# Kernel optimization log

Hardware: AMD Instinct MI355X
Metric: run time of the kernel (lower is better)

## Reference

```python
import jax, jax.numpy as jnp
import numpy as np

SCALES = [1, 2, 4, 8]
NB_CODE = 1024
CODE_DIM = 512


def _linear_upsample(x, t_out):
    """torch F.interpolate(mode='linear', align_corners=False) on last axis. x: [N, C, t_in]."""
    t_in = x.shape[-1]
    if t_in == t_out:
        return x
    pos = (jnp.arange(t_out, dtype=x.dtype) + 0.5) * (t_in / t_out) - 0.5
    pos = jnp.clip(pos, 0.0, t_in - 1)
    lo = jnp.floor(pos).astype(jnp.int32)
    hi = jnp.minimum(lo + 1, t_in - 1)
    w = (pos - lo.astype(x.dtype))
    return x[..., lo] * (1.0 - w) + x[..., hi] * w


def setup_inputs() -> dict:
    key = jax.random.key(0)
    k1, k2 = jax.random.split(key)
    x = jax.random.normal(k1, (16, CODE_DIM, 2048), dtype=jnp.float32)
    codebook = jax.random.normal(k2, (NB_CODE, CODE_DIM), dtype=jnp.float32) * 0.02
    return {"x": x, "codebook": codebook}


def reference(x, codebook):
    # Eval-mode forward of HRQuantizeEMAReset: hierarchical residual VQ.
    # temperature=0 -> deterministic nearest-code argmax; m_lens=None -> full mask.
    N, C, T = x.shape
    residual = x
    f_hat = jnp.zeros_like(x)
    mean_vq_loss = jnp.asarray(0.0, dtype=x.dtype)
    csq = jnp.sum(codebook ** 2, axis=-1)  # [K]
    all_idx = []
    for scale in SCALES:
        t_s = T // scale
        # area downsample == average pooling over non-overlapping windows
        rest_down = residual if scale == 1 else residual.reshape(N, C, t_s, scale).mean(-1)
        flat = rest_down.transpose(0, 2, 1).reshape(N * t_s, C)  # (n t) c
        # squared-euclidean distance to all codes via GEMM
        dist = (jnp.sum(flat ** 2, axis=-1, keepdims=True)
                - 2.0 * flat @ codebook.T + csq[None, :])  # [N*t_s, K]
        code_idx = jnp.argmin(dist, axis=-1)  # gumbel_sample with temp=0
        all_idx.append(code_idx)
        x_d = codebook[code_idx].reshape(N, t_s, C).transpose(0, 2, 1)  # [N, C, t_s]
        up_x_d = _linear_upsample(x_d, T)
        residual = residual - up_x_d
        f_hat = f_hat + up_x_d
        # per-scale commitment loss against running reconstruction (detached)
        mean_vq_loss = mean_vq_loss + jnp.mean((x - jax.lax.stop_gradient(f_hat)) ** 2)
    mean_vq_loss = mean_vq_loss / len(SCALES)
    # straight-through estimator
    f_hat = x + jax.lax.stop_gradient(f_hat - x)
    # perplexity over all codes used across scales
    codes = jnp.concatenate(all_idx)
    counts = jnp.zeros((NB_CODE,), dtype=x.dtype).at[codes].add(1.0)
    prob = counts / jnp.sum(counts)
    perplexity = jnp.exp(-jnp.sum(prob * jnp.log(prob + 1e-7)))
    return f_hat, mean_vq_loss, perplexity
```

## Files before the change

kernel.cpp:

```cpp
#include <hip/hip_runtime.h>

#define CDIM 512
#define TDIM 2048
#define KCODE 1024
#define NTOT 16
#define FH_ELEMS (NTOT * CDIM * TDIM)
#define M_TOTAL 61440

typedef unsigned long long u64;
typedef unsigned int u32;
typedef __attribute__((ext_vector_type(8))) short s16x8;
typedef __attribute__((ext_vector_type(4))) float f32x4;
typedef __attribute__((ext_vector_type(4))) int i32x4;
typedef __attribute__((ext_vector_type(2))) int i32x2;

__device__ __forceinline__ u64 umin64(u64 a, u64 b) { return a < b ? a : b; }

__device__ __forceinline__ u32 bf16_rne(float f) {
  u32 u = __float_as_uint(f);
  return (u + 0x7fffu + ((u >> 16) & 1u)) >> 16;
}
__device__ __forceinline__ u32 pack2ch(float v0, float v1) {
  return bf16_rne(v0) | (bf16_rne(v1) << 16);
}
__device__ __forceinline__ int tile_addr(int ml, int kbyte) {
  return (ml * 128 + kbyte) ^ ((ml & 7) << 4);
}
__device__ __forceinline__ int iclamp(int v, int lo, int hi) {
  return v < lo ? lo : (v > hi ? hi : v);
}

__global__ __launch_bounds__(64) void csq_kernel(const float* __restrict__ cb,
                                                 float* __restrict__ csq) {
  const int code = blockIdx.x;
  const int t = threadIdx.x;
  const float* row = cb + (size_t)code * CDIM;
  float s = 0.f;
#pragma unroll
  for (int q = 0; q < 2; ++q) {
    float4 v = *(const float4*)(row + (t * 2 + q) * 4);
    s += v.x * v.x + v.y * v.y + v.z * v.z + v.w * v.w;
  }
#pragma unroll
  for (int off = 32; off; off >>= 1) s += __shfl_down(s, off, 64);
  if (t == 0) csq[code] = s;
}

__global__ __launch_bounds__(256) void cbprep_kernel(const float* __restrict__ cb,
                                                     char* __restrict__ cb_pack) {
  const int g = blockIdx.x * 256 + threadIdx.x;
  const int tile = g >> 10;
  const int L = (g & 1023) * 16;
  const int nt = tile >> 3, kc = tile & 7;
  const int code_local = L >> 7;
  const int kbyte = (L & 127) ^ ((code_local & 7) << 4);
  const int code = nt * 128 + code_local;
  const int c0 = kc * 64 + (kbyte >> 1);
  f32x4 va = *(const f32x4*)(cb + (size_t)code * CDIM + c0);
  f32x4 vb = *(const f32x4*)(cb + (size_t)code * CDIM + c0 + 4);
  i32x4 o = {(int)pack2ch(va[0], va[1]), (int)pack2ch(va[2], va[3]),
             (int)pack2ch(vb[0], vb[1]), (int)pack2ch(vb[2], vb[3])};
  *(i32x4*)(cb_pack + (size_t)g * 16) = o;
}

__global__ __launch_bounds__(256) void xprep_kernel(const float* __restrict__ x,
                                                    char* __restrict__ a1) {
  const int tid = threadIdx.x;
  const int lane = tid & 63, cq = tid >> 6;
  const int blk = blockIdx.x;
  const int tb = blk & 7;
  const int kc = (blk >> 3) & 7;
  const int n = blk >> 6;
  const int c0 = kc * 64 + cq * 16;
  const int t0 = tb * 256 + lane * 4;
  const float* xp = x + (size_t)n * (CDIM * TDIM) + (size_t)c0 * TDIM + t0;
  u32 pk[4][8];
#pragma unroll
  for (int jp = 0; jp < 8; ++jp) {
    f32x4 v0 = *(const f32x4*)(xp + (size_t)(2 * jp) * TDIM);
    f32x4 v1 = *(const f32x4*)(xp + (size_t)(2 * jp + 1) * TDIM);
#pragma unroll
    for (int tt = 0; tt < 4; ++tt) pk[tt][jp] = pack2ch(v0[tt], v1[tt]);
  }
  const int kbyte = cq * 32;
#pragma unroll
  for (int tt = 0; tt < 4; ++tt) {
    const int m = n * TDIM + t0 + tt;
    const size_t tbase = ((size_t)((m >> 7) * 8 + kc)) << 14;
    i32x4 o1 = {(int)pk[tt][0], (int)pk[tt][1], (int)pk[tt][2], (int)pk[tt][3]};
    i32x4 o2 = {(int)pk[tt][4], (int)pk[tt][5], (int)pk[tt][6], (int)pk[tt][7]};
    *(i32x4*)(a1 + tbase + tile_addr(m & 127, kbyte)) = o1;
    *(i32x4*)(a1 + tbase + tile_addr(m & 127, kbyte + 16)) = o2;
  }
}

__global__ __launch_bounds__(512, 2) void gemm_argmin_packed(
    const char* __restrict__ a_pack,
    const char* __restrict__ cb_pack,
    const float* __restrict__ csq,
    u64* __restrict__ packed) {
  __shared__ __align__(16) char smem[131072 + 1024];
  float* csq_s = (float*)(smem + 131072);

  const int id = blockIdx.x;
  const int nxq = gridDim.x >> 5;
  const int xcd = id & 7;
  const int rr = id >> 3;
  const int bx = xcd * nxq + (rr >> 2);
  const int by = rr & 3;

  const int tid = threadIdx.x;
  const int lane = tid & 63;
  const int w = tid >> 6;
  const int wc = w >> 2;
  const int wm = w & 3;
  const int row_base = bx * 256;
  const int code_base = by * 256;
  if (tid < 256) csq_s[tid] = csq[code_base + tid];

  const f32x4 zero = {0.f, 0.f, 0.f, 0.f};
  f32x4 acc[8][4];
#pragma unroll
  for (int fc = 0; fc < 8; ++fc)
#pragma unroll
    for (int fm = 0; fm < 4; ++fm) acc[fc][fm] = zero;

  const size_t aBase = ((size_t)(bx * 2) * 8) << 14;
  const size_t bBase = ((size_t)(by * 2) * 8) << 14;

  auto stage = [&](int buf, int kc) {
    char* dst = smem + buf * 65536;
    const char* gA0 = a_pack + aBase + ((size_t)kc << 14);
    const char* gA1 = a_pack + aBase + ((size_t)(8 + kc) << 14);
    const char* gB0 = cb_pack + bBase + ((size_t)kc << 14);
    const char* gB1 = cb_pack + bBase + ((size_t)(8 + kc) << 14);
    const int o = tid * 16;
#pragma unroll
    for (int p = 0; p < 2; ++p) {
      const int q = o + p * 8192;
      __builtin_amdgcn_global_load_lds(
          (const __attribute__((address_space(1))) u32*)(gA0 + q),
          (__attribute__((address_space(3))) u32*)(dst + q), 16, 0, 0);
      __builtin_amdgcn_global_load_lds(
          (const __attribute__((address_space(1))) u32*)(gA1 + q),
          (__attribute__((address_space(3))) u32*)(dst + 16384 + q), 16, 0, 0);
      __builtin_amdgcn_global_load_lds(
          (const __attribute__((address_space(1))) u32*)(gB0 + q),
          (__attribute__((address_space(3))) u32*)(dst + 32768 + q), 16, 0, 0);
      __builtin_amdgcn_global_load_lds(
          (const __attribute__((address_space(1))) u32*)(gB1 + q),
          (__attribute__((address_space(3))) u32*)(dst + 49152 + q), 16, 0, 0);
    }
  };

  stage(0, 0);
  __syncthreads();

  int cur = 0;
  for (int kc = 0; kc < 8; ++kc) {
    if (kc < 7) stage(cur ^ 1, kc + 1);
    const char* X = smem + cur * 65536;
    const char* C = X + 32768;
#pragma unroll
    for (int ks = 0; ks < 2; ++ks) {
      const int kb = ks * 64 + (lane >> 4) * 16;
      s16x8 af[8], bq[4];
#pragma unroll
      for (int fc = 0; fc < 8; ++fc) {
        const int cr = wc * 128 + fc * 16 + (lane & 15);
        af[fc] = *(const s16x8*)(C + ((cr >> 7) << 14) +
                                 tile_addr(cr & 127, kb));
      }
#pragma unroll
      for (int fm = 0; fm < 4; ++fm) {
        const int mr = wm * 64 + fm * 16 + (lane & 15);
        bq[fm] = *(const s16x8*)(X + ((mr >> 7) << 14) +
                                 tile_addr(mr & 127, kb));
      }
      __builtin_amdgcn_s_setprio(1);
#pragma unroll
      for (int fc = 0; fc < 8; ++fc)
#pragma unroll
        for (int fm = 0; fm < 4; ++fm)
          acc[fc][fm] = __builtin_amdgcn_mfma_f32_16x16x32_bf16(
              af[fc], bq[fm], acc[fc][fm], 0, 0, 0);
      __builtin_amdgcn_s_setprio(0);
    }
    __syncthreads();
    cur ^= 1;
  }

  u64 best[4] = {~0ull, ~0ull, ~0ull, ~0ull};
#pragma unroll
  for (int fc = 0; fc < 8; ++fc) {
#pragma unroll
    for (int r4 = 0; r4 < 4; ++r4) {
      const int cl = wc * 128 + fc * 16 + (lane >> 4) * 4 + r4;
      const float cs = csq_s[cl];
      const u64 codebits = (u32)(code_base + cl);
#pragma unroll
      for (int fm = 0; fm < 4; ++fm) {
        float d = fmaf(-2.0f, acc[fc][fm][r4], cs);
        u32 u = __float_as_uint(d);
        u = (u & 0x80000000u) ? ~u : (u | 0x80000000u);
        best[fm] = umin64(best[fm], ((u64)u << 32) | codebits);
      }
    }
  }
#pragma unroll
  for (int fm = 0; fm < 4; ++fm) {
    u64 b = best[fm];
#pragma unroll
    for (int off = 16; off < 64; off <<= 1) {
      u32 lo = (u32)b, hi = (u32)(b >> 32);
      lo = (u32)__shfl_xor((int)lo, off, 64);
      hi = (u32)__shfl_xor((int)hi, off, 64);
      b = umin64(b, ((u64)hi << 32) | lo);
    }
    if ((lane >> 4) == 0)
      atomicMin(&packed[row_base + wm * 64 + fm * 16 + (lane & 15)], b);
  }
}

__global__ __launch_bounds__(256) void pack2_kernel(
    const float* __restrict__ x, const float* __restrict__ cb,
    const u64* __restrict__ packed, char* __restrict__ a2,
    float* __restrict__ poolr2) {
  __shared__ float rows1[16][516];
  __shared__ int idx1[16];
  const int tid = threadIdx.x;
  const int blk = blockIdx.x;
  const int n = blk >> 7;
  const int tau0 = (blk & 127) * 8;
  const int tb = tau0 * 2;
  if (tid < 16)
    idx1[tid] = (int)(packed[(size_t)n * TDIM + tb + tid] & 0xffffffffull);
  __syncthreads();
  {
    const int rj = tid >> 4, c16 = tid & 15;
    const float* src = cb + (size_t)idx1[rj] * CDIM;
#pragma unroll
    for (int q = 0; q < 8; ++q) {
      const int c = c16 * 4 + q * 64;
      *(f32x4*)&rows1[rj][c] = *(const f32x4*)(src + c);
    }
  }
  __syncthreads();

  const int cg = tid >> 1, half = tid & 1;
  const int c0 = cg * 4;
  const int tl0 = half * 8;
  const size_t xbase =
      (size_t)n * (CDIM * TDIM) + (size_t)c0 * TDIM + tb + tl0;

  f32x4 ru[8];
#pragma unroll
  for (int t = 0; t < 8; ++t) ru[t] = *(const f32x4*)&rows1[tl0 + t][c0];

  float p2[4][4];
#pragma unroll
  for (int j = 0; j < 4; ++j) {
    f32x4 xa = *(const f32x4*)(x + xbase + (size_t)j * TDIM);
    f32x4 xb = *(const f32x4*)(x + xbase + (size_t)j * TDIM + 4);
#pragma unroll
    for (int q = 0; q < 4; ++q) {
      const float e0 = (q < 2) ? xa[2 * q] : xb[2 * q - 4];
      const float e1 = (q < 2) ? xa[2 * q + 1] : xb[2 * q - 3];
      const float r0 = e0 - ru[2 * q][j];
      const float r1 = e1 - ru[2 * q + 1][j];
      p2[j][q] = (r0 + r1) * 0.5f;
    }
  }
#pragma unroll
  for (int q = 0; q < 4; ++q) {
    f32x4 o = {p2[0][q], p2[1][q], p2[2][q], p2[3][q]};
    *(f32x4*)(poolr2 + (size_t)n * (1024 * CDIM) +
              (size_t)(tau0 + half * 4 + q) * CDIM + c0) = o;
  }
  const int kc = c0 >> 6, kbyte = (c0 & 63) * 2;
#pragma unroll
  for (int q = 0; q < 4; ++q) {
    const int m = n * 1024 + tau0 + half * 4 + q;
    i32x2 o = {(int)pack2ch(p2[0][q], p2[1][q]),
               (int)pack2ch(p2[2][q], p2[3][q])};
    *(i32x2*)(a2 + (((size_t)((m >> 7) * 8 + kc)) << 14) +
              tile_addr(m & 127, kbyte)) = o;
  }
}

template <int TP, bool WPOOL>
__global__ __launch_bounds__(256) void packN_kernel(
    const float* __restrict__ pin, const float* __restrict__ cb,
    const u64* __restrict__ packed, char* __restrict__ a_next,
    float* __restrict__ pout) {
  constexpr int OFF = (TP == 1024) ? 32768 : 49152;
  constexpr int TILES = TP / 16;
  constexpr int TO = TP / 2;
  __shared__ float rows[18][516];
  __shared__ int idxs[18];
  const int tid = threadIdx.x;
  const int blk = blockIdx.x;
  const int n = blk / TILES;
  const int o0 = (blk % TILES) * 8;
  const int s0 = o0 * 2;
  if (tid < 18) {
    const int sig = iclamp(s0 - 1 + tid, 0, TP - 1);
    idxs[tid] = (int)(packed[OFF + (size_t)n * TP + sig] & 0xffffffffull);
  }
  __syncthreads();
  for (int j = 0; j < 18; ++j) {
    const int c = tid * 2;
    const float* src = cb + (size_t)idxs[j] * CDIM + c;
    rows[j][c] = src[0];
    rows[j][c + 1] = src[1];
  }
  __syncthreads();

  const int cg = tid >> 1, half = tid & 1;
  const int c0 = cg * 4;
  f32x4 inv[8];
#pragma unroll
  for (int l = 0; l < 8; ++l)
    inv[l] = *(const f32x4*)(pin + (size_t)n * (TP * CDIM) +
                             (size_t)(s0 + half * 8 + l) * CDIM + c0);

  float pv[4][4];
#pragma unroll
  for (int q = 0; q < 4; ++q) {
    const int e = half * 8 + 2 * q;
    const int sa = e + 1, sb = e + 2;
    f32x4 Rm = *(const f32x4*)&rows[sa - 1][c0];
    f32x4 Rc = *(const f32x4*)&rows[sa][c0];
    f32x4 Rp = *(const f32x4*)&rows[sb][c0];
    f32x4 Rpp = *(const f32x4*)&rows[sb + 1][c0];
    f32x4 ua = 0.125f * (Rm + Rp) + 0.75f * Rc;
    f32x4 ub = 0.125f * (Rc + Rpp) + 0.75f * Rp;
#pragma unroll
    for (int j = 0; j < 4; ++j)
      pv[j][q] = ((inv[2 * q][j] - ua[j]) + (inv[2 * q + 1][j] - ub[j])) * 0.5f;
  }

  if constexpr (WPOOL) {
#pragma unroll
    for (int q = 0; q < 4; ++q) {
      f32x4 o = {pv[0][q], pv[1][q], pv[2][q], pv[3][q]};
      *(f32x4*)(pout + (size_t)n * (TO * CDIM) +
                (size_t)(o0 + half * 4 + q) * CDIM + c0) = o;
    }
  }
  const int kc = c0 >> 6, kbyte = (c0 & 63) * 2;
#pragma unroll
  for (int q = 0; q < 4; ++q) {
    const int m = n * TO + o0 + half * 4 + q;
    i32x2 o = {(int)pack2ch(pv[0][q], pv[1][q]),
               (int)pack2ch(pv[2][q], pv[3][q])};
    *(i32x2*)(a_next + (((size_t)((m >> 7) * 8 + kc)) << 14) +
              tile_addr(m & 127, kbyte)) = o;
  }
}

__global__ __launch_bounds__(256) void final_kernel(
    const float* __restrict__ x, float* __restrict__ out,
    const float* __restrict__ cb, const u64* __restrict__ packed,
    float* __restrict__ lossPart) {
  __shared__ float red[4];
  const int tid = threadIdx.x;
  const int blk = blockIdx.x;
  const int ch = blk & 1;
  const int t0 = ((blk >> 1) & 127) * 16;
  const int n = blk >> 8;
  const int cg = tid >> 2, qt = tid & 3;
  const int c0 = ch * 256 + cg * 4;
  const int tb = t0 + qt * 4;

  const u64* ip1 = packed + (size_t)n * TDIM;
  const u64* ip2 = packed + 32768 + (size_t)n * 1024;
  const u64* ip4 = packed + 49152 + (size_t)n * 512;
  const u64* ip8 = packed + 57344 + (size_t)n * 256;

  f32x4 R1[4], R2[4], R4[3], R8[2];
#pragma unroll
  for (int k = 0; k < 4; ++k)
    R1[k] = *(const f32x4*)(
        cb + (size_t)(u32)(ip1[tb + k] & 0xffffffffull) * CDIM + c0);
  const int b2 = tb >> 1;
#pragma unroll
  for (int k = 0; k < 4; ++k) {
    const int s = iclamp(b2 - 1 + k, 0, 1023);
    R2[k] = *(const f32x4*)(
        cb + (size_t)(u32)(ip2[s] & 0xffffffffull) * CDIM + c0);
  }
  const int b4 = tb >> 2;
#pragma unroll
  for (int k = 0; k < 3; ++k) {
    const int s = iclamp(b4 - 1 + k, 0, 511);
    R4[k] = *(const f32x4*)(
        cb + (size_t)(u32)(ip4[s] & 0xffffffffull) * CDIM + c0);
  }
  const int b8 = (tb >> 3) - 1 + ((tb >> 2) & 1);
#pragma unroll
  for (int k = 0; k < 2; ++k) {
    const int s = iclamp(b8 + k, 0, 255);
    R8[k] = *(const f32x4*)(
        cb + (size_t)(u32)(ip8[s] & 0xffffffffull) * CDIM + c0);
  }

  const size_t xbase = (size_t)n * (CDIM * TDIM) + (size_t)c0 * TDIM + tb;
  f32x4 xa[4], fa[4];
#pragma unroll
  for (int j = 0; j < 4; ++j)
    xa[j] = *(const f32x4*)(x + xbase + (size_t)j * TDIM);

  const int s2n[4] = {0, 1, 1, 2};
  const float w2n[4] = {0.75f, 0.25f, 0.75f, 0.25f};
  const int s4n[4] = {0, 0, 1, 1};
  const float w4n[4] = {0.625f, 0.875f, 0.125f, 0.375f};
  const float w8base = (tb & 4) ? 0.0625f : 0.5625f;

  float ss1 = 0.f, ss2 = 0.f, ss3 = 0.f, ss4 = 0.f;
#pragma unroll
  for (int tt = 0; tt < 4; ++tt) {
    f32x4 u2 = R2[s2n[tt]] * (1.f - w2n[tt]) + R2[s2n[tt] + 1] * w2n[tt];
    f32x4 u4 = R4[s4n[tt]] * (1.f - w4n[tt]) + R4[s4n[tt] + 1] * w4n[tt];
    const float w8 = w8base + tt * 0.125f;
    f32x4 u8 = R8[0] * (1.f - w8) + R8[1] * w8;
    f32x4 xv;
#pragma unroll
    for (int j = 0; j < 4; ++j) xv[j] = xa[j][tt];
    f32x4 r1 = xv - R1[tt];
    f32x4 r2 = r1 - u2;
    f32x4 r3 = r2 - u4;
    f32x4 r4 = r3 - u8;
#pragma unroll
    for (int j = 0; j < 4; ++j) {
      ss1 += r1[j] * r1[j];
      ss2 += r2[j] * r2[j];
      ss3 += r3[j] * r3[j];
      ss4 += r4[j] * r4[j];
    }
    f32x4 fh = xv - r4;
#pragma unroll
    for (int j = 0; j < 4; ++j) fa[j][tt] = fh[j];
  }
#pragma unroll
  for (int j = 0; j < 4; ++j)
    *(f32x4*)(out + xbase + (size_t)j * TDIM) = fa[j];

  __shared__ float red2[4][4];
  float sv[4] = {ss1, ss2, ss3, ss4};
  const int w = tid >> 6, lane = tid & 63;
#pragma unroll
  for (int st = 0; st < 4; ++st) {
    float v = sv[st];
#pragma unroll
    for (int off = 32; off; off >>= 1) v += __shfl_down(v, off, 64);
    if (lane == 0) red2[w][st] = v;
  }
  __syncthreads();
  if (tid < 4)
    lossPart[tid * 4096 + blk] =
        red2[0][tid] + red2[1][tid] + red2[2][tid] + red2[3][tid];
  (void)red;
}

__global__ __launch_bounds__(256) void hist_kernel(const u64* __restrict__ packed,
                                                   int* __restrict__ hist) {
  const int i = blockIdx.x * 256 + threadIdx.x;
  const int code = (int)(packed[i] & 0xFFFFFFFFull);
  atomicAdd(&hist[code], 1);
}

__global__ __launch_bounds__(256) void finalize_kernel(
    const float* __restrict__ lossPart, const int* __restrict__ hist,
    float* __restrict__ outTail) {
  __shared__ float red[4];
  const int tid = threadIdx.x;
  float s = 0.f;
  for (int i = tid; i < 4 * 4096; i += 256) s += lossPart[i];
#pragma unroll
  for (int off = 32; off; off >>= 1) s += __shfl_down(s, off, 64);
  if ((tid & 63) == 0) red[tid >> 6] = s;
  __syncthreads();
  const float loss =
      (red[0] + red[1] + red[2] + red[3]) * (1.0f / (4.0f * 16777216.0f));
  __syncthreads();
  float e = 0.f;
  for (int k = tid; k < KCODE; k += 256) {
    float p = (float)hist[k] * (1.0f / 61440.0f);
    e += p * logf(p + 1e-7f);
  }
#pragma unroll
  for (int off = 32; off; off >>= 1) e += __shfl_down(e, off, 64);
  if ((tid & 63) == 0) red[tid >> 6] = e;
  __syncthreads();
  if (tid == 0) {
    outTail[0] = loss;
    outTail[1] = expf(-(red[0] + red[1] + red[2] + red[3]));
  }
}

extern "C" void kernel_launch(void* const* d_in, const int* in_sizes, int n_in,
                              void* d_out, int out_size, void* d_ws,
                              size_t ws_size, hipStream_t stream) {
  const float* x = (const float*)d_in[0];
  const float* cb = (const float*)d_in[1];
  float* out = (float*)d_out;

  char* ws = (char*)d_ws;
  u64* packed = (u64*)ws;
  float* csq = (float*)(ws + 491520);
  int* hist = (int*)(ws + 495616);
  float* lossPart = (float*)(ws + 499712);
  char* cb_pack = ws + 565248;
  char* a2 = ws + (2ull << 20);
  char* a4 = ws + (18ull << 20);
  char* a8 = ws + (26ull << 20);

  hipMemsetAsync(packed, 0xFF, (size_t)M_TOTAL * 8, stream);
  hipMemsetAsync(hist, 0, KCODE * sizeof(int), stream);
  csq_kernel<<<KCODE, 64, 0, stream>>>(cb, csq);
  cbprep_kernel<<<256, 256, 0, stream>>>(cb, cb_pack);

  u64* p1 = packed;
  u64* p2 = packed + 32768;
  u64* p4 = packed + 49152;
  u64* p8 = packed + 57344;

  char* a1 = (char*)out;
  float* poolr2 = out;
  float* poolr4 = out + 8388608;

  xprep_kernel<<<1024, 256, 0, stream>>>(x, a1);
  gemm_argmin_packed<<<128 * 4, 512, 0, stream>>>(a1, cb_pack, csq, p1);
  pack2_kernel<<<2048, 256, 0, stream>>>(x, cb, packed, a2, poolr2);
  gemm_argmin_packed<<<64 * 4, 512, 0, stream>>>(a2, cb_pack, csq, p2);
  packN_kernel<1024, true>
      <<<1024, 256, 0, stream>>>(poolr2, cb, packed, a4, poolr4);
  gemm_argmin_packed<<<32 * 4, 512, 0, stream>>>(a4, cb_pack, csq, p4);
  packN_kernel<512, false>
      <<<512, 256, 0, stream>>>(poolr4, cb, packed, a8, nullptr);
  gemm_argmin_packed<<<16 * 4, 512, 0, stream>>>(a8, cb_pack, csq, p8);
  final_kernel<<<4096, 256, 0, stream>>>(x, out, cb, packed, lossPart);

  hist_kernel<<<240, 256, 0, stream>>>(packed, hist);
  finalize_kernel<<<1, 256, 0, stream>>>(lossPart, hist, out + FH_ELEMS);
}
```

Baseline: 247.6 us.

## Restructure pack kernels to channel-major pooled layout with direct codebook gathers

Rewrites pack2 and packN so each wave covers 256 time steps for 4 channels, reading codebook rows straight from global memory instead of staging them in shared memory. The intermediate pooled residual buffers switch from time-major to channel-major so reads and writes along time are coalesced. Blocks are remapped with a chunked swizzle of block IDs, pack2 launches twice as many blocks, and final_kernel gets the same wave/lane-to-(time, channel) mapping. The aim is to remove LDS staging and barriers and improve coalescing, at the cost of more scattered 16-byte codebook gathers through cache.

```diff
diff --git a/kernel.cpp b/kernel.cpp
--- a/kernel.cpp
+++ b/kernel.cpp
@@ -11,6 +11,7 @@
 typedef unsigned int u32;
 typedef __attribute__((ext_vector_type(8))) short s16x8;
 typedef __attribute__((ext_vector_type(4))) float f32x4;
+typedef __attribute__((ext_vector_type(2))) float f32x2;
 typedef __attribute__((ext_vector_type(4))) int i32x4;
 typedef __attribute__((ext_vector_type(2))) int i32x2;
 
@@ -28,6 +29,9 @@
 }
 __device__ __forceinline__ int iclamp(int v, int lo, int hi) {
   return v < lo ? lo : (v > hi ? hi : v);
+}
+__device__ __forceinline__ int swz_chunk(int b, int nblk) {
+  return (b & 7) * (nblk >> 3) + (b >> 3);
 }
 
 __global__ __launch_bounds__(64) void csq_kernel(const float* __restrict__ cb,
@@ -226,61 +230,45 @@
     const float* __restrict__ x, const float* __restrict__ cb,
     const u64* __restrict__ packed, char* __restrict__ a2,
     float* __restrict__ poolr2) {
-  __shared__ float rows1[16][516];
-  __shared__ int idx1[16];
   const int tid = threadIdx.x;
-  const int blk = blockIdx.x;
-  const int n = blk >> 7;
-  const int tau0 = (blk & 127) * 8;
-  const int tb = tau0 * 2;
-  if (tid < 16)
-    idx1[tid] = (int)(packed[(size_t)n * TDIM + tb + tid] & 0xffffffffull);
-  __syncthreads();
-  {
-    const int rj = tid >> 4, c16 = tid & 15;
-    const float* src = cb + (size_t)idx1[rj] * CDIM;
-#pragma unroll
-    for (int q = 0; q < 8; ++q) {
-      const int c = c16 * 4 + q * 64;
-      *(f32x4*)&rows1[rj][c] = *(const f32x4*)(src + c);
-    }
-  }
-  __syncthreads();
-
-  const int cg = tid >> 1, half = tid & 1;
-  const int c0 = cg * 4;
-  const int tl0 = half * 8;
-  const size_t xbase =
-      (size_t)n * (CDIM * TDIM) + (size_t)c0 * TDIM + tb + tl0;
-
-  f32x4 ru[8];
-#pragma unroll
-  for (int t = 0; t < 8; ++t) ru[t] = *(const f32x4*)&rows1[tl0 + t][c0];
-
-  float p2[4][4];
+  const int w = tid >> 6, lane = tid & 63;
+  const int L = swz_chunk(blockIdx.x, gridDim.x);
+  const int cbk = L & 31;
+  const int tt = (L >> 5) & 7;
+  const int n = L >> 8;
+  const int c0 = cbk * 16 + w * 4;
+  const int tb = tt * 256 + lane * 4;
+  const int tau0 = tb >> 1;
+
+  const u64* ip1 = packed + (size_t)n * TDIM;
+  f32x4 R1[4];
+#pragma unroll
+  for (int k = 0; k < 4; ++k)
+    R1[k] = *(const f32x4*)(
+        cb + (size_t)(u32)(ip1[tb + k] & 0xffffffffull) * CDIM + c0);
+
+  const size_t xbase = (size_t)n * (CDIM * TDIM) + (size_t)c0 * TDIM + tb;
+  float p2[4][2];
 #pragma unroll
   for (int j = 0; j < 4; ++j) {
     f32x4 xa = *(const f32x4*)(x + xbase + (size_t)j * TDIM);
-    f32x4 xb = *(const f32x4*)(x + xbase + (size_t)j * TDIM + 4);
-#pragma unroll
-    for (int q = 0; q < 4; ++q) {
-      const float e0 = (q < 2) ? xa[2 * q] : xb[2 * q - 4];
-      const float e1 = (q < 2) ? xa[2 * q + 1] : xb[2 * q - 3];
-      const float r0 = e0 - ru[2 * q][j];
-      const float r1 = e1 - ru[2 * q + 1][j];
+#pragma unroll
+    for (int q = 0; q < 2; ++q) {
+      const float r0 = xa[2 * q] - R1[2 * q][j];
+      const float r1 = xa[2 * q + 1] - R1[2 * q + 1][j];
       p2[j][q] = (r0 + r1) * 0.5f;
     }
   }
 #pragma unroll
-  for (int q = 0; q < 4; ++q) {
-    f32x4 o = {p2[0][q], p2[1][q], p2[2][q], p2[3][q]};
-    *(f32x4*)(poolr2 + (size_t)n * (1024 * CDIM) +
-              (size_t)(tau0 + half * 4 + q) * CDIM + c0) = o;
+  for (int j = 0; j < 4; ++j) {
+    f32x2 o = {p2[j][0], p2[j][1]};
+    *(f32x2*)(poolr2 + (size_t)n * (CDIM * 1024) + (size_t)(c0 + j) * 1024 +
+              tau0) = o;
   }
   const int kc = c0 >> 6, kbyte = (c0 & 63) * 2;
 #pragma unroll
-  for (int q = 0; q < 4; ++q) {
-    const int m = n * 1024 + tau0 + half * 4 + q;
+  for (int q = 0; q < 2; ++q) {
+    const int m = n * 1024 + tau0 + q;
     i32x2 o = {(int)pack2ch(p2[0][q], p2[1][q]),
                (int)pack2ch(p2[2][q], p2[3][q])};
     *(i32x2*)(a2 + (((size_t)((m >> 7) * 8 + kc)) << 14) +
@@ -294,64 +282,64 @@
     const u64* __restrict__ packed, char* __restrict__ a_next,
     float* __restrict__ pout) {
   constexpr int OFF = (TP == 1024) ? 32768 : 49152;
-  constexpr int TILES = TP / 16;
   constexpr int TO = TP / 2;
-  __shared__ float rows[18][516];
-  __shared__ int idxs[18];
   const int tid = threadIdx.x;
-  const int blk = blockIdx.x;
-  const int n = blk / TILES;
-  const int o0 = (blk % TILES) * 8;
-  const int s0 = o0 * 2;
-  if (tid < 18) {
-    const int sig = iclamp(s0 - 1 + tid, 0, TP - 1);
-    idxs[tid] = (int)(packed[OFF + (size_t)n * TP + sig] & 0xffffffffull);
-  }
-  __syncthreads();
-  for (int j = 0; j < 18; ++j) {
-    const int c = tid * 2;
-    const float* src = cb + (size_t)idxs[j] * CDIM + c;
-    rows[j][c] = src[0];
-    rows[j][c + 1] = src[1];
-  }
-  __syncthreads();
-
-  const int cg = tid >> 1, half = tid & 1;
-  const int c0 = cg * 4;
-  f32x4 inv[8];
-#pragma unroll
-  for (int l = 0; l < 8; ++l)
-    inv[l] = *(const f32x4*)(pin + (size_t)n * (TP * CDIM) +
-                             (size_t)(s0 + half * 8 + l) * CDIM + c0);
+  const int w = tid >> 6, lane = tid & 63;
+  const int L = swz_chunk(blockIdx.x, gridDim.x);
+  const int cbk = L & 31;
+  int n, o0;
+  if constexpr (TP == 1024) {
+    const int th = (L >> 5) & 1;
+    n = L >> 6;
+    o0 = th * 256 + lane * 4;
+  } else {
+    n = L >> 5;
+    o0 = lane * 4;
+  }
+  const int c0 = cbk * 16 + w * 4;
+  const int s0 = 2 * o0;
+
+  const u64* ip = packed + OFF + (size_t)n * TP;
+  f32x4 R[10];
+#pragma unroll
+  for (int j = 0; j < 10; ++j) {
+    const int s = iclamp(s0 - 1 + j, 0, TP - 1);
+    R[j] = *(const f32x4*)(
+        cb + (size_t)(u32)(ip[s] & 0xffffffffull) * CDIM + c0);
+  }
+  f32x4 ina[4], inb[4];
+#pragma unroll
+  for (int j = 0; j < 4; ++j) {
+    const float* p = pin + (size_t)n * (CDIM * TP) + (size_t)(c0 + j) * TP + s0;
+    ina[j] = *(const f32x4*)p;
+    inb[j] = *(const f32x4*)(p + 4);
+  }
 
   float pv[4][4];
 #pragma unroll
   for (int q = 0; q < 4; ++q) {
-    const int e = half * 8 + 2 * q;
-    const int sa = e + 1, sb = e + 2;
-    f32x4 Rm = *(const f32x4*)&rows[sa - 1][c0];
-    f32x4 Rc = *(const f32x4*)&rows[sa][c0];
-    f32x4 Rp = *(const f32x4*)&rows[sb][c0];
-    f32x4 Rpp = *(const f32x4*)&rows[sb + 1][c0];
-    f32x4 ua = 0.125f * (Rm + Rp) + 0.75f * Rc;
-    f32x4 ub = 0.125f * (Rc + Rpp) + 0.75f * Rp;
-#pragma unroll
-    for (int j = 0; j < 4; ++j)
-      pv[j][q] = ((inv[2 * q][j] - ua[j]) + (inv[2 * q + 1][j] - ub[j])) * 0.5f;
+    f32x4 ua = 0.125f * (R[2 * q] + R[2 * q + 2]) + 0.75f * R[2 * q + 1];
+    f32x4 ub = 0.125f * (R[2 * q + 1] + R[2 * q + 3]) + 0.75f * R[2 * q + 2];
+#pragma unroll
+    for (int j = 0; j < 4; ++j) {
+      const int l = 2 * q;
+      const float ia = (l < 4) ? ina[j][l] : inb[j][l - 4];
+      const float ib = (l + 1 < 4) ? ina[j][l + 1] : inb[j][l - 3];
+      pv[j][q] = ((ia - ua[j]) + (ib - ub[j])) * 0.5f;
+    }
   }
 
   if constexpr (WPOOL) {
 #pragma unroll
-    for (int q = 0; q < 4; ++q) {
-      f32x4 o = {pv[0][q], pv[1][q], pv[2][q], pv[3][q]};
-      *(f32x4*)(pout + (size_t)n * (TO * CDIM) +
-                (size_t)(o0 + half * 4 + q) * CDIM + c0) = o;
+    for (int j = 0; j < 4; ++j) {
+      f32x4 o = {pv[j][0], pv[j][1], pv[j][2], pv[j][3]};
+      *(f32x4*)(pout + (size_t)n * (CDIM * TO) + (size_t)(c0 + j) * TO + o0) = o;
     }
   }
   const int kc = c0 >> 6, kbyte = (c0 & 63) * 2;
 #pragma unroll
   for (int q = 0; q < 4; ++q) {
-    const int m = n * TO + o0 + half * 4 + q;
+    const int m = n * TO + o0 + q;
     i32x2 o = {(int)pack2ch(pv[0][q], pv[1][q]),
                (int)pack2ch(pv[2][q], pv[3][q])};
     *(i32x2*)(a_next + (((size_t)((m >> 7) * 8 + kc)) << 14) +
@@ -363,15 +351,14 @@
     const float* __restrict__ x, float* __restrict__ out,
     const float* __restrict__ cb, const u64* __restrict__ packed,
     float* __restrict__ lossPart) {
-  __shared__ float red[4];
   const int tid = threadIdx.x;
+  const int w = tid >> 6, lane = tid & 63;
   const int blk = blockIdx.x;
-  const int ch = blk & 1;
-  const int t0 = ((blk >> 1) & 127) * 16;
+  const int tt = blk & 7;
+  const int cbk = (blk >> 3) & 31;
   const int n = blk >> 8;
-  const int cg = tid >> 2, qt = tid & 3;
-  const int c0 = ch * 256 + cg * 4;
-  const int tb = t0 + qt * 4;
+  const int c0 = cbk * 16 + w * 4;
+  const int tb = tt * 256 + lane * 4;
 
   const u64* ip1 = packed + (size_t)n * TDIM;
   const u64* ip2 = packed + 32768 + (size_t)n * 1024;
@@ -419,15 +406,15 @@
 
   float ss1 = 0.f, ss2 = 0.f, ss3 = 0.f, ss4 = 0.f;
 #pragma unroll
-  for (int tt = 0; tt < 4; ++tt) {
-    f32x4 u2 = R2[s2n[tt]] * (1.f - w2n[tt]) + R2[s2n[tt] + 1] * w2n[tt];
-    f32x4 u4 = R4[s4n[tt]] * (1.f - w4n[tt]) + R4[s4n[tt] + 1] * w4n[tt];
-    const float w8 = w8base + tt * 0.125f;
+  for (int tt2 = 0; tt2 < 4; ++tt2) {
+    f32x4 u2 = R2[s2n[tt2]] * (1.f - w2n[tt2]) + R2[s2n[tt2] + 1] * w2n[tt2];
+    f32x4 u4 = R4[s4n[tt2]] * (1.f - w4n[tt2]) + R4[s4n[tt2] + 1] * w4n[tt2];
+    const float w8 = w8base + tt2 * 0.125f;
     f32x4 u8 = R8[0] * (1.f - w8) + R8[1] * w8;
     f32x4 xv;
 #pragma unroll
-    for (int j = 0; j < 4; ++j) xv[j] = xa[j][tt];
-    f32x4 r1 = xv - R1[tt];
+    for (int j = 0; j < 4; ++j) xv[j] = xa[j][tt2];
+    f32x4 r1 = xv - R1[tt2];
     f32x4 r2 = r1 - u2;
     f32x4 r3 = r2 - u4;
     f32x4 r4 = r3 - u8;
@@ -440,7 +427,7 @@
     }
     f32x4 fh = xv - r4;
 #pragma unroll
-    for (int j = 0; j < 4; ++j) fa[j][tt] = fh[j];
+    for (int j = 0; j < 4; ++j) fa[j][tt2] = fh[j];
   }
 #pragma unroll
   for (int j = 0; j < 4; ++j)
@@ -448,7 +435,6 @@
 
   __shared__ float red2[4][4];
   float sv[4] = {ss1, ss2, ss3, ss4};
-  const int w = tid >> 6, lane = tid & 63;
 #pragma unroll
   for (int st = 0; st < 4; ++st) {
     float v = sv[st];
@@ -460,7 +446,6 @@
   if (tid < 4)
     lossPart[tid * 4096 + blk] =
         red2[0][tid] + red2[1][tid] + red2[2][tid] + red2[3][tid];
-  (void)red;
 }
 
 __global__ __launch_bounds__(256) void hist_kernel(const u64* __restrict__ packed,
@@ -532,7 +517,7 @@
 
   xprep_kernel<<<1024, 256, 0, stream>>>(x, a1);
   gemm_argmin_packed<<<128 * 4, 512, 0, stream>>>(a1, cb_pack, csq, p1);
-  pack2_kernel<<<2048, 256, 0, stream>>>(x, cb, packed, a2, poolr2);
+  pack2_kernel<<<4096, 256, 0, stream>>>(x, cb, packed, a2, poolr2);
   gemm_argmin_packed<<<64 * 4, 512, 0, stream>>>(a2, cb_pack, csq, p2);
   packN_kernel<1024, true>
       <<<1024, 256, 0, stream>>>(poolr2, cb, packed, a4, poolr4);
```

Result: slower. 263.4 us (+6.4%).
